# Kernel tuning notes

Hardware: AMD Instinct MI355X
Metric: run time of the kernel (lower is better)

The kernel has to match this reference:

```python
import jax, jax.numpy as jnp
import numpy as np

N = 100000
E = 1600000
D_IN = 128
H1 = 128
H2 = 128
C = 64


def setup_inputs() -> dict:
    key = jax.random.key(0)
    ks = jax.random.split(key, 10)
    x_content = jax.random.normal(ks[0], (N, D_IN), dtype=jnp.float32)
    edge_index = jax.random.randint(ks[1], (2, E), 0, N, dtype=jnp.int64)
    # SAGEConv params: lin_l (applied to aggregated neighbors, has bias),
    # lin_r (applied to root node, no bias). Kaiming-ish scaling.
    def lin(k, fan_in, fan_out):
        return jax.random.normal(k, (fan_in, fan_out), dtype=jnp.float32) / np.sqrt(fan_in)
    return {
        "x_content": x_content,
        "edge_index": edge_index,
        "W1l": lin(ks[2], D_IN, H1),
        "b1": jnp.zeros((H1,), jnp.float32),
        "W1r": lin(ks[3], D_IN, H1),
        "W2l": lin(ks[4], H1, H2),
        "b2": jnp.zeros((H2,), jnp.float32),
        "W2r": lin(ks[5], H1, H2),
        "Wout": lin(ks[6], H2, C),
        "bout": jnp.zeros((C,), jnp.float32),
    }


def _sage_conv(x, src, dst, Wl, b, Wr):
    # mean-aggregate neighbor features (messages flow src -> dst), then
    # out = mean_agg @ Wl + b + x @ Wr  (PyG SAGEConv, aggr='mean')
    msgs = x[src]                                            # [E, d]
    agg = jax.ops.segment_sum(msgs, dst, num_segments=N)     # [N, d]
    deg = jax.ops.segment_sum(jnp.ones((src.shape[0],), x.dtype), dst, num_segments=N)
    mean = agg / jnp.clip(deg, 1.0)[:, None]
    return mean @ Wl + b + x @ Wr


def reference(x_content, edge_index, W1l, b1, W1r, W2l, b2, W2r, Wout, bout):
    src, dst = edge_index[0], edge_index[1]
    # dropout is identity in eval mode (training=False)
    x = jax.nn.relu(_sage_conv(x_content, src, dst, W1l, b1, W1r))
    x = jax.nn.relu(_sage_conv(x, src, dst, W2l, b2, W2r))
    return x @ Wout + bout
```

## Files before the change

### kernel.cpp

```cpp
#include <hip/hip_runtime.h>
#include <hip/hip_fp8.h>

#define DD 128
#define CC 64
#define BKW 512
#define NPB 4096

typedef __attribute__((ext_vector_type(8))) short short8v;
typedef __attribute__((ext_vector_type(4))) float f32x4;
typedef __attribute__((ext_vector_type(2))) float f32x2;

static __device__ inline ushort f2bf_rne(float f) {
    unsigned u = __float_as_uint(f);
    unsigned r = (u + 0x7FFFu + ((u >> 16) & 1u)) >> 16;
    return (ushort)r;
}
static __device__ inline float bf2f(ushort h) {
    return __uint_as_float(((unsigned)h) << 16);
}
static __device__ inline float bflo(uint u) {
    return __uint_as_float(u << 16);
}
static __device__ inline float bfhi(uint u) {
    return __uint_as_float(u & 0xffff0000u);
}

__global__ __launch_bounds__(256) void bucket_cnt_kernel(const int* __restrict__ ei,
                                                         int* __restrict__ bcnt, int E) {
    __shared__ int h[256];
    const int t = threadIdx.x;
    h[t] = 0;
    __syncthreads();
    const int base = blockIdx.x * 8192;
    const int end = min(E, base + 8192);
    for (int j = base + t; j < end; j += 256) {
        atomicAdd(&h[ei[E + j] >> 9], 1);
    }
    __syncthreads();
    if (h[t]) atomicAdd(&bcnt[t], h[t]);
}

__global__ __launch_bounds__(256) void bucket_scan_kernel(const int* __restrict__ bcnt,
                                                          int* __restrict__ boffs,
                                                          int* __restrict__ bcur) {
    __shared__ int s[256];
    const int t = threadIdx.x;
    int v = bcnt[t];
    s[t] = v;
    __syncthreads();
    for (int off = 1; off < 256; off <<= 1) {
        int xv = 0;
        if (t >= off) xv = s[t - off];
        __syncthreads();
        if (t >= off) s[t] += xv;
        __syncthreads();
    }
    int excl = s[t] - v;
    boffs[t] = excl;
    bcur[t] = excl;
    if (t == 255) boffs[256] = s[255];
}

__global__ __launch_bounds__(256) void binA_kernel(const int* __restrict__ ei,
                                                   int* __restrict__ bcur,
                                                   uint* __restrict__ ebuf, int E) {
    __shared__ int sRun[256];
    __shared__ int sRel[256];
    __shared__ int sBase[256];
    __shared__ uint sPair[NPB];
    __shared__ unsigned char sBkt[NPB];
    __shared__ int sHist[256];
    const int t = threadIdx.x;
    const int e0 = blockIdx.x * NPB;
    const int cntE = min(NPB, E - e0);

    sHist[t] = 0;
    __syncthreads();
    for (int j = t; j < cntE; j += 256) {
        int dst = ei[E + e0 + j];
        atomicAdd(&sHist[dst >> 9], 1);
    }
    __syncthreads();
    int h = sHist[t];
    sRun[t] = h;
    __syncthreads();
    for (int off = 1; off < 256; off <<= 1) {
        int v = 0;
        if (t >= off) v = sRun[t - off];
        __syncthreads();
        if (t >= off) sRun[t] += v;
        __syncthreads();
    }
    int runstart = sRun[t] - h;
    int base = 0;
    if (h > 0) base = atomicAdd(&bcur[t], h);
    sRun[t] = runstart;
    sRel[t] = runstart;
    sBase[t] = base;
    __syncthreads();
    for (int j = t; j < cntE; j += 256) {
        int src = ei[e0 + j];
        int dst = ei[E + e0 + j];
        int b = dst >> 9;
        int slot = atomicAdd(&sRel[b], 1);
        sPair[slot] = (uint)src | ((uint)(dst & 511) << 17);
        sBkt[slot] = (unsigned char)b;
    }
    __syncthreads();
    for (int s = t; s < cntE; s += 256) {
        uint p = sPair[s];
        int b = (int)sBkt[s];
        int gpos = sBase[b] + (s - sRun[b]);
        ebuf[gpos] = p;
    }
}

__global__ __launch_bounds__(256) void binB2_kernel(const uint* __restrict__ ebuf,
                                                    const int* __restrict__ boffs,
                                                    int* __restrict__ offs,
                                                    int* __restrict__ csr, int n) {
    __shared__ int sCnt[BKW];
    __shared__ int sOffs[BKW];
    __shared__ int sScan[256];
    const int t = threadIdx.x;
    const int node0 = blockIdx.x * BKW;
    const int node1 = min(n, node0 + BKW);
    const int start = boffs[blockIdx.x];
    const int end = boffs[blockIdx.x + 1];

    sCnt[t] = 0; sCnt[t + 256] = 0;
    __syncthreads();
    for (int j = start + t; j < end; j += 256) {
        int d = (int)(ebuf[j] >> 17);
        atomicAdd(&sCnt[d], 1);
    }
    __syncthreads();
    int v0 = sCnt[2 * t], v1 = sCnt[2 * t + 1];
    int sum = v0 + v1;
    sScan[t] = sum;
    __syncthreads();
    for (int off = 1; off < 256; off <<= 1) {
        int xv = 0;
        if (t >= off) xv = sScan[t - off];
        __syncthreads();
        if (t >= off) sScan[t] += xv;
        __syncthreads();
    }
    int excl = sScan[t] - sum;
    sOffs[2 * t] = start + excl;
    sOffs[2 * t + 1] = start + excl + v0;
    __syncthreads();
    for (int i = t; i < BKW; i += 256) {
        int node = node0 + i;
        if (node < n) offs[node] = sOffs[i];
    }
    if (node1 == n && t == 0) offs[n] = end;
    __syncthreads();
    sCnt[t] = 0; sCnt[t + 256] = 0;
    __syncthreads();
    for (int j = start + t; j < end; j += 256) {
        uint p = ebuf[j];
        int d = (int)(p >> 17);
        int r = atomicAdd(&sCnt[d], 1);
        csr[sOffs[d] + r] = (int)(p & 0x1FFFFu);
    }
}

__global__ __launch_bounds__(256) void prep_kernel(
    const float* __restrict__ x, ushort* __restrict__ xh, uint* __restrict__ xq,
    const float* __restrict__ Wl1, const float* __restrict__ Wr1,
    const float* __restrict__ Wl2, const float* __restrict__ Wr2,
    const float* __restrict__ Wout,
    ushort* __restrict__ WTfrag1, ushort* __restrict__ WTfrag2,
    ushort* __restrict__ WoFrag, int nxblk) {
    const int t = threadIdx.x;
    const int bx = blockIdx.x;
    if (bx < nxblk) {
        int i = bx * 256 + t;
        float4 a = ((const float4*)x)[2 * i];
        float4 b = ((const float4*)x)[2 * i + 1];
        float vv[8] = {a.x, a.y, a.z, a.w, b.x, b.y, b.z, b.w};
        ushort r[8];
        uint q[8];
        #pragma unroll
        for (int j = 0; j < 8; ++j) {
            r[j] = f2bf_rne(vv[j]);
            q[j] = (uint)__hip_fp8_e4m3(vv[j]).__x;
        }
        uint4 o;
        o.x = (uint)r[0] | ((uint)r[1] << 16);
        o.y = (uint)r[2] | ((uint)r[3] << 16);
        o.z = (uint)r[4] | ((uint)r[5] << 16);
        o.w = (uint)r[6] | ((uint)r[7] << 16);
        ((uint4*)xh)[i] = o;
        uint2 oq;
        oq.x = q[0] | (q[1] << 8) | (q[2] << 16) | (q[3] << 24);
        oq.y = q[4] | (q[5] << 8) | (q[6] << 16) | (q[7] << 24);
        ((uint2*)xq)[i] = oq;
    } else if (bx < nxblk + 32) {
        int li = bx - nxblk;
        int layer = li >> 4;
        int idx = (li & 15) * 256 + t;
        const float* Wl = layer ? Wl2 : Wl1;
        const float* Wr = layer ? Wr2 : Wr1;
        ushort* dst = (layer ? WTfrag2 : WTfrag1) + (size_t)idx * 8;
        int lane = idx & 63, tt = (idx >> 6) & 7, s = idx >> 9;
        int col = tt * 16 + (lane & 15);
        int k0 = s * 32 + (lane >> 4) * 8;
        #pragma unroll
        for (int j = 0; j < 8; ++j) {
            int k = k0 + j;
            float v = (k < DD) ? Wl[k * DD + col] : Wr[(k - DD) * DD + col];
            dst[j] = f2bf_rne(v);
        }
    } else {
        int idx = (bx - nxblk - 32) * 256 + t;
        ushort* dst = WoFrag + (size_t)idx * 8;
        int lane = idx & 63, tt = (idx >> 6) & 3, kc = idx >> 8;
        int col = tt * 16 + (lane & 15);
        int k0 = kc * 32 + (lane >> 4) * 8;
        #pragma unroll
        for (int j = 0; j < 8; ++j) {
            dst[j] = f2bf_rne(Wout[(k0 + j) * CC + col]);
        }
    }
}

__global__ __launch_bounds__(256) void csr_agg8_kernel(
    const uint* __restrict__ xq, const int* __restrict__ offs,
    const int* __restrict__ csr, ushort* __restrict__ meanH, int n) {
    int node = blockIdx.x * 4 + (threadIdx.x >> 6);
    if (node >= n) return;
    const int lane = threadIdx.x & 63;
    const int sub = lane >> 4;
    const int li = lane & 15;
    const int start = offs[node];
    const int c = offs[node + 1] - start;
    f32x2 a[4], aa[4];
    #pragma unroll
    for (int k = 0; k < 4; ++k) { a[k] = (f32x2){0.f, 0.f}; aa[k] = (f32x2){0.f, 0.f}; }
    #define ACC8(A, U) { \
        A[0] += __builtin_amdgcn_cvt_pk_f32_fp8(U.x, false); \
        A[1] += __builtin_amdgcn_cvt_pk_f32_fp8(U.x, true);  \
        A[2] += __builtin_amdgcn_cvt_pk_f32_fp8(U.y, false); \
        A[3] += __builtin_amdgcn_cvt_pk_f32_fp8(U.y, true);  }
    const int c16 = c & ~15;
    int j = 0;
    if (c16 > 0) {
        int s0 = csr[start + sub];
        int s1 = csr[start + 4 + sub];
        int s2 = csr[start + 8 + sub];
        int s3 = csr[start + 12 + sub];
        for (; j < c16; j += 16) {
            int t0 = 0, t1 = 0, t2 = 0, t3 = 0;
            if (j + 16 < c16) {
                t0 = csr[start + j + 16 + sub];
                t1 = csr[start + j + 20 + sub];
                t2 = csr[start + j + 24 + sub];
                t3 = csr[start + j + 28 + sub];
            }
            uint2 u0 = *(const uint2*)((const uchar*)xq + (size_t)s0 * DD + li * 8);
            uint2 u1 = *(const uint2*)((const uchar*)xq + (size_t)s1 * DD + li * 8);
            uint2 u2 = *(const uint2*)((const uchar*)xq + (size_t)s2 * DD + li * 8);
            uint2 u3 = *(const uint2*)((const uchar*)xq + (size_t)s3 * DD + li * 8);
            ACC8(a, u0); ACC8(a, u1); ACC8(aa, u2); ACC8(aa, u3);
            s0 = t0; s1 = t1; s2 = t2; s3 = t3;
        }
    }
    if (c - j >= 8) {
        int s0 = csr[start + j + sub];
        int s1 = csr[start + j + 4 + sub];
        uint2 u0 = *(const uint2*)((const uchar*)xq + (size_t)s0 * DD + li * 8);
        uint2 u1 = *(const uint2*)((const uchar*)xq + (size_t)s1 * DD + li * 8);
        ACC8(a, u0); ACC8(aa, u1);
        j += 8;
    }
    if (c - j >= 4) {
        int s = csr[start + j + sub];
        uint2 u = *(const uint2*)((const uchar*)xq + (size_t)s * DD + li * 8);
        ACC8(a, u);
        j += 4;
    }
    if (j + sub < c) {
        int s = csr[start + j + sub];
        uint2 u = *(const uint2*)((const uchar*)xq + (size_t)s * DD + li * 8);
        ACC8(aa, u);
    }
    #undef ACC8
    float res[8];
    #pragma unroll
    for (int k = 0; k < 4; ++k) {
        f32x2 v = a[k] + aa[k];
        float e0 = v.x; e0 += __shfl_xor(e0, 16); e0 += __shfl_xor(e0, 32);
        float e1 = v.y; e1 += __shfl_xor(e1, 16); e1 += __shfl_xor(e1, 32);
        res[2 * k] = e0; res[2 * k + 1] = e1;
    }
    if (sub == 0) {
        float inv = 1.0f / fmaxf((float)c, 1.0f);
        short8v o;
        #pragma unroll
        for (int k = 0; k < 8; ++k) o[k] = (short)f2bf_rne(res[k] * inv);
        *(short8v*)(meanH + (size_t)node * DD + li * 8) = o;
    }
}

template <bool PROJ>
__global__ __launch_bounds__(256) void layer_mfma_kernel(
    const ushort* __restrict__ meanH, const ushort* __restrict__ rootH,
    const ushort* __restrict__ WTfrag, const float* __restrict__ bias,
    ushort* __restrict__ outH, uchar* __restrict__ outQ,
    const ushort* __restrict__ WoFrag, const float* __restrict__ bout,
    float* __restrict__ outF, int n) {
    __shared__ ushort sH[PROJ ? 64 : 1][136];
    const int tid = threadIdx.x;
    const int w = tid >> 6;
    const int l = tid & 63;
    const int row0 = blockIdx.x * 64;
    const int lrow = w * 16 + (l & 15);
    const int kb = (l >> 4) * 8;
    const int lcol = l & 15;
    const int arowg = min(row0 + lrow, n - 1);

    const ushort* Am = meanH + (size_t)arowg * DD;
    const ushort* Ar = rootH + (size_t)arowg * DD;

    short8v ap[8];
    #pragma unroll
    for (int s = 0; s < 8; ++s) {
        ap[s] = (s < 4) ? *(const short8v*)(Am + s * 32 + kb)
                        : *(const short8v*)(Ar + (s - 4) * 32 + kb);
    }

    f32x4 acc[8];
    #pragma unroll
    for (int t = 0; t < 8; ++t) acc[t] = (f32x4){0.f, 0.f, 0.f, 0.f};

    #pragma unroll
    for (int s = 0; s < 8; ++s) {
        const ushort* fb = WTfrag + (size_t)s * 4096 + l * 8;
        #pragma unroll
        for (int t = 0; t < 8; ++t) {
            short8v bh = *(const short8v*)(fb + t * 512);
            acc[t] = __builtin_amdgcn_mfma_f32_16x16x32_bf16(ap[s], bh, acc[t], 0, 0, 0);
        }
    }

    const int lrow0 = w * 16 + (l >> 4) * 4;
    if (!PROJ) {
        #pragma unroll
        for (int t = 0; t < 8; ++t) {
            const int col = t * 16 + lcol;
            const float b = bias[col];
            #pragma unroll
            for (int r = 0; r < 4; ++r) {
                int row = row0 + lrow0 + r;
                if (row < n) {
                    float o = fmaxf(acc[t][r] + b, 0.f);
                    outH[(size_t)row * DD + col] = f2bf_rne(o);
                    outQ[(size_t)row * DD + col] = __hip_fp8_e4m3(o).__x;
                }
            }
        }
    } else {
        #pragma unroll
        for (int t = 0; t < 8; ++t) {
            const int col = t * 16 + lcol;
            const float b = bias[col];
            #pragma unroll
            for (int r = 0; r < 4; ++r) {
                sH[lrow0 + r][col] = f2bf_rne(fmaxf(acc[t][r] + b, 0.f));
            }
        }
        __syncthreads();
        f32x4 po[4];
        #pragma unroll
        for (int t = 0; t < 4; ++t) po[t] = (f32x4){0.f, 0.f, 0.f, 0.f};
        #pragma unroll
        for (int kc = 0; kc < 4; ++kc) {
            short8v ah = *(const short8v*)&sH[lrow][kc * 32 + kb];
            const ushort* fb = WoFrag + (size_t)kc * 2048 + l * 8;
            #pragma unroll
            for (int t = 0; t < 4; ++t) {
                short8v bh = *(const short8v*)(fb + t * 512);
                po[t] = __builtin_amdgcn_mfma_f32_16x16x32_bf16(ah, bh, po[t], 0, 0, 0);
            }
        }
        #pragma unroll
        for (int t = 0; t < 4; ++t) {
            const int col = t * 16 + lcol;
            const float b = bout[col];
            #pragma unroll
            for (int r = 0; r < 4; ++r) {
                int row = row0 + lrow0 + r;
                if (row < n) outF[(size_t)row * CC + col] = po[t][r] + b;
            }
        }
    }
}

extern "C" void kernel_launch(void* const* d_in, const int* in_sizes, int n_in,
                              void* d_out, int out_size, void* d_ws, size_t ws_size,
                              hipStream_t stream) {
    const float* x    = (const float*)d_in[0];
    const int*   ei   = (const int*)d_in[1];
    const float* W1l  = (const float*)d_in[2];
    const float* b1   = (const float*)d_in[3];
    const float* W1r  = (const float*)d_in[4];
    const float* W2l  = (const float*)d_in[5];
    const float* b2   = (const float*)d_in[6];
    const float* W2r  = (const float*)d_in[7];
    const float* Wout = (const float*)d_in[8];
    const float* bout = (const float*)d_in[9];
    float* out = (float*)d_out;
    const int n = in_sizes[0] / DD;
    const int E = in_sizes[1] / 2;
    const size_t NP = (size_t)n * DD;

    const int NBUCK = (n + BKW - 1) / BKW;

    int* offs  = (int*)d_ws;
    int* bcnt  = offs + 100352;
    int* boffs = bcnt + 256;
    int* bcur  = boffs + 512;
    int* csr   = bcur + 256;
    uint* ebuf = (uint*)(csr + 1600256);
    uint* xq   = ebuf;
    ushort* xh = (ushort*)((uchar*)xq + NP);
    ushort* meanH = xh + NP;
    ushort* h1h = meanH + NP;
    ushort* WTfrag1 = h1h + NP;
    ushort* WTfrag2 = WTfrag1 + 32768;
    ushort* WoFrag  = WTfrag2 + 32768;
    uchar* h1q = (uchar*)(WoFrag + 8192);

    hipMemsetAsync(bcnt, 0, sizeof(int) * 256, stream);
    bucket_cnt_kernel<<<(E + 8191) / 8192, 256, 0, stream>>>(ei, bcnt, E);
    bucket_scan_kernel<<<1, 256, 0, stream>>>(bcnt, boffs, bcur);
    binA_kernel<<<(E + NPB - 1) / NPB, 256, 0, stream>>>(ei, bcur, ebuf, E);
    binB2_kernel<<<NBUCK, 256, 0, stream>>>(ebuf, boffs, offs, csr, n);

    const int nxblk = (int)(NP / 8 / 256);
    prep_kernel<<<nxblk + 36, 256, 0, stream>>>(x, xh, xq, W1l, W1r, W2l, W2r,
                                                Wout, WTfrag1, WTfrag2, WoFrag, nxblk);

    const int nblk = (n + 63) / 64;
    const int ablk = (n + 3) / 4;

    csr_agg8_kernel<<<ablk, 256, 0, stream>>>(xq, offs, csr, meanH, n);
    layer_mfma_kernel<false><<<nblk, 256, 0, stream>>>(
        meanH, xh, WTfrag1, b1, h1h, h1q,
        (const ushort*)nullptr, (const float*)nullptr, (float*)nullptr, n);

    csr_agg8_kernel<<<ablk, 256, 0, stream>>>((const uint*)h1q, offs, csr, meanH, n);
    layer_mfma_kernel<true><<<nblk, 256, 0, stream>>>(
        meanH, h1h, WTfrag2, b2, (ushort*)nullptr, (uchar*)nullptr,
        WoFrag, bout, out, n);
}
```

Before: 234.1 us.

## Make layer GEMM persistent with register-resident weights and LDS-staged coalesced stores

The dense layer kernel becomes persistent, with 625 blocks looping over 32-row tiles. Each wave keeps its half of the weight fragments (64 output columns) in registers for the whole kernel, so weights are no longer re-read from memory for every tile. Layer-1 outputs, in bf16 and fp8, are staged through LDS and written back as 16-byte coalesced stores instead of scattered 2-byte and 1-byte stores. The cost is heavy register pressure from holding 32 short8 fragments per lane, which may lower occupancy, plus extra syncthreads per tile.

After: 227.1 us. -3.0%, faster.

```diff
diff --git a/kernel.cpp b/kernel.cpp
--- a/kernel.cpp
+++ b/kernel.cpp
@@ -17,12 +17,6 @@
 }
 static __device__ inline float bf2f(ushort h) {
     return __uint_as_float(((unsigned)h) << 16);
-}
-static __device__ inline float bflo(uint u) {
-    return __uint_as_float(u << 16);
-}
-static __device__ inline float bfhi(uint u) {
-    return __uint_as_float(u & 0xffff0000u);
 }
 
 __global__ __launch_bounds__(256) void bucket_cnt_kernel(const int* __restrict__ ei,
@@ -310,90 +304,117 @@
     const ushort* __restrict__ WTfrag, const float* __restrict__ bias,
     ushort* __restrict__ outH, uchar* __restrict__ outQ,
     const ushort* __restrict__ WoFrag, const float* __restrict__ bout,
-    float* __restrict__ outF, int n) {
-    __shared__ ushort sH[PROJ ? 64 : 1][136];
+    float* __restrict__ outF, int n, int ntiles) {
+    __shared__ ushort sH[32][136];
+    __shared__ uchar sQ[PROJ ? 1 : 32][PROJ ? 16 : 144];
     const int tid = threadIdx.x;
     const int w = tid >> 6;
     const int l = tid & 63;
-    const int row0 = blockIdx.x * 64;
-    const int lrow = w * 16 + (l & 15);
+    const int rh = w >> 1;
+    const int ch = w & 1;
+    const int lrow = rh * 16 + (l & 15);
     const int kb = (l >> 4) * 8;
     const int lcol = l & 15;
-    const int arowg = min(row0 + lrow, n - 1);
-
-    const ushort* Am = meanH + (size_t)arowg * DD;
-    const ushort* Ar = rootH + (size_t)arowg * DD;
-
-    short8v ap[8];
+    const int lrow0 = rh * 16 + (l >> 4) * 4;
+
+    short8v breg[8][4];
     #pragma unroll
     for (int s = 0; s < 8; ++s) {
-        ap[s] = (s < 4) ? *(const short8v*)(Am + s * 32 + kb)
-                        : *(const short8v*)(Ar + (s - 4) * 32 + kb);
-    }
-
-    f32x4 acc[8];
+        #pragma unroll
+        for (int t = 0; t < 4; ++t) {
+            breg[s][t] = *(const short8v*)(WTfrag + (size_t)s * 4096 +
+                                           (ch * 4 + t) * 512 + l * 8);
+        }
+    }
+    float bias_r[4];
     #pragma unroll
-    for (int t = 0; t < 8; ++t) acc[t] = (f32x4){0.f, 0.f, 0.f, 0.f};
-
-    #pragma unroll
-    for (int s = 0; s < 8; ++s) {
-        const ushort* fb = WTfrag + (size_t)s * 4096 + l * 8;
-        #pragma unroll
-        for (int t = 0; t < 8; ++t) {
-            short8v bh = *(const short8v*)(fb + t * 512);
-            acc[t] = __builtin_amdgcn_mfma_f32_16x16x32_bf16(ap[s], bh, acc[t], 0, 0, 0);
-        }
-    }
-
-    const int lrow0 = w * 16 + (l >> 4) * 4;
-    if (!PROJ) {
-        #pragma unroll
-        for (int t = 0; t < 8; ++t) {
-            const int col = t * 16 + lcol;
-            const float b = bias[col];
-            #pragma unroll
-            for (int r = 0; r < 4; ++r) {
-                int row = row0 + lrow0 + r;
-                if (row < n) {
-                    float o = fmaxf(acc[t][r] + b, 0.f);
-                    outH[(size_t)row * DD + col] = f2bf_rne(o);
-                    outQ[(size_t)row * DD + col] = __hip_fp8_e4m3(o).__x;
-                }
-            }
-        }
-    } else {
-        #pragma unroll
-        for (int t = 0; t < 8; ++t) {
-            const int col = t * 16 + lcol;
-            const float b = bias[col];
-            #pragma unroll
-            for (int r = 0; r < 4; ++r) {
-                sH[lrow0 + r][col] = f2bf_rne(fmaxf(acc[t][r] + b, 0.f));
-            }
-        }
-        __syncthreads();
-        f32x4 po[4];
-        #pragma unroll
-        for (int t = 0; t < 4; ++t) po[t] = (f32x4){0.f, 0.f, 0.f, 0.f};
-        #pragma unroll
-        for (int kc = 0; kc < 4; ++kc) {
-            short8v ah = *(const short8v*)&sH[lrow][kc * 32 + kb];
-            const ushort* fb = WoFrag + (size_t)kc * 2048 + l * 8;
+    for (int t = 0; t < 4; ++t) bias_r[t] = bias[ch * 64 + t * 16 + lcol];
+
+    for (int tile = blockIdx.x; tile < ntiles; tile += gridDim.x) {
+        const int row0 = tile * 32;
+        const int arowg = min(row0 + lrow, n - 1);
+        const ushort* Am = meanH + (size_t)arowg * DD;
+        const ushort* Ar = rootH + (size_t)arowg * DD;
+        short8v ap[8];
+        #pragma unroll
+        for (int s = 0; s < 8; ++s) {
+            ap[s] = (s < 4) ? *(const short8v*)(Am + s * 32 + kb)
+                            : *(const short8v*)(Ar + (s - 4) * 32 + kb);
+        }
+        f32x4 acc[4];
+        #pragma unroll
+        for (int t = 0; t < 4; ++t) acc[t] = (f32x4){0.f, 0.f, 0.f, 0.f};
+        #pragma unroll
+        for (int s = 0; s < 8; ++s) {
             #pragma unroll
             for (int t = 0; t < 4; ++t) {
-                short8v bh = *(const short8v*)(fb + t * 512);
-                po[t] = __builtin_amdgcn_mfma_f32_16x16x32_bf16(ah, bh, po[t], 0, 0, 0);
-            }
-        }
-        #pragma unroll
-        for (int t = 0; t < 4; ++t) {
-            const int col = t * 16 + lcol;
-            const float b = bout[col];
+                acc[t] = __builtin_amdgcn_mfma_f32_16x16x32_bf16(ap[s], breg[s][t],
+                                                                 acc[t], 0, 0, 0);
+            }
+        }
+
+        if (!PROJ) {
             #pragma unroll
-            for (int r = 0; r < 4; ++r) {
-                int row = row0 + lrow0 + r;
-                if (row < n) outF[(size_t)row * CC + col] = po[t][r] + b;
-            }
+            for (int t = 0; t < 4; ++t) {
+                const int col = ch * 64 + t * 16 + lcol;
+                #pragma unroll
+                for (int r = 0; r < 4; ++r) {
+                    float o = fmaxf(acc[t][r] + bias_r[t], 0.f);
+                    sH[lrow0 + r][col] = f2bf_rne(o);
+                    sQ[lrow0 + r][col] = __hip_fp8_e4m3(o).__x;
+                }
+            }
+            __syncthreads();
+            for (int i = tid; i < 512; i += 256) {
+                int row = i >> 4, seg = i & 15;
+                int grow = row0 + row;
+                if (grow < n)
+                    *(uint4*)(outH + (size_t)grow * DD + seg * 8) =
+                        *(const uint4*)&sH[row][seg * 8];
+            }
+            {
+                int row = tid >> 3, seg = tid & 7;
+                int grow = row0 + row;
+                if (grow < n)
+                    *(uint4*)(outQ + (size_t)grow * DD + seg * 16) =
+                        *(const uint4*)&sQ[row][seg * 16];
+            }
+            __syncthreads();
+        } else {
+            #pragma unroll
+            for (int t = 0; t < 4; ++t) {
+                const int col = ch * 64 + t * 16 + lcol;
+                #pragma unroll
+                for (int r = 0; r < 4; ++r) {
+                    sH[lrow0 + r][col] = f2bf_rne(fmaxf(acc[t][r] + bias_r[t], 0.f));
+                }
+            }
+            __syncthreads();
+            f32x4 po[2];
+            po[0] = (f32x4){0.f, 0.f, 0.f, 0.f};
+            po[1] = (f32x4){0.f, 0.f, 0.f, 0.f};
+            #pragma unroll
+            for (int kc = 0; kc < 4; ++kc) {
+                short8v ah = *(const short8v*)&sH[lrow][kc * 32 + kb];
+                #pragma unroll
+                for (int t2 = 0; t2 < 2; ++t2) {
+                    short8v bh = *(const short8v*)(WoFrag + (size_t)kc * 2048 +
+                                                   (ch * 2 + t2) * 512 + l * 8);
+                    po[t2] = __builtin_amdgcn_mfma_f32_16x16x32_bf16(ah, bh,
+                                                                     po[t2], 0, 0, 0);
+                }
+            }
+            #pragma unroll
+            for (int t2 = 0; t2 < 2; ++t2) {
+                const int col = ch * 32 + t2 * 16 + lcol;
+                const float b = bout[col];
+                #pragma unroll
+                for (int r = 0; r < 4; ++r) {
+                    int grow = row0 + lrow0 + r;
+                    if (grow < n) outF[(size_t)grow * CC + col] = po[t2][r] + b;
+                }
+            }
+            __syncthreads();
         }
     }
 }
@@ -443,16 +464,17 @@
     prep_kernel<<<nxblk + 36, 256, 0, stream>>>(x, xh, xq, W1l, W1r, W2l, W2r,
                                                 Wout, WTfrag1, WTfrag2, WoFrag, nxblk);
 
-    const int nblk = (n + 63) / 64;
+    const int ntiles = (n + 31) / 32;
+    const int lgrid = 625;
     const int ablk = (n + 3) / 4;
 
     csr_agg8_kernel<<<ablk, 256, 0, stream>>>(xq, offs, csr, meanH, n);
-    layer_mfma_kernel<false><<<nblk, 256, 0, stream>>>(
+    layer_mfma_kernel<false><<<lgrid, 256, 0, stream>>>(
         meanH, xh, WTfrag1, b1, h1h, h1q,
-        (const ushort*)nullptr, (const float*)nullptr, (float*)nullptr, n);
+        (const ushort*)nullptr, (const float*)nullptr, (float*)nullptr, n, ntiles);
 
     csr_agg8_kernel<<<ablk, 256, 0, stream>>>((const uint*)h1q, offs, csr, meanH, n);
-    layer_mfma_kernel<true><<<nblk, 256, 0, stream>>>(
+    layer_mfma_kernel<true><<<lgrid, 256, 0, stream>>>(
         meanH, h1h, WTfrag2, b2, (ushort*)nullptr, (uchar*)nullptr,
-        WoFrag, bout, out, n);
-}
+        WoFrag, bout, out, n, ntiles);
+}
```
